# Kernel optimization log

Measured on AMD Instinct MI355X. Metric: run time of the kernel, lower is better.

The kernel has to match this reference:

```python
import jax, jax.numpy as jnp
import numpy as np

DIM, K_RANK, L, N_CLASS = 64, 16, 8, 10
H = 1e-3
B = 256
DD = DIM * DIM  # 4096


def _cay(C, D):
    # Cayley transform of B = C @ D^T : I + C (I - 0.5 D^T C)^{-1} D^T
    Id = jnp.eye(C.shape[1], dtype=C.dtype)
    DT = jnp.swapaxes(D, 1, 2)
    inv = jnp.linalg.inv(Id - 0.5 * DT @ C)
    return Id + C @ inv @ DT


def setup_inputs() -> dict:
    key = jax.random.key(0)
    ks = jax.random.split(key, 9)
    u = jax.random.normal(ks[0], (B, DIM, K_RANK), jnp.float32) / np.float32(np.sqrt(DIM))
    vh = jax.random.normal(ks[1], (B, K_RANK, DIM), jnp.float32) / np.float32(np.sqrt(DIM))
    eye_k = jnp.eye(K_RANK, dtype=jnp.float32)
    off = 0.05 * jax.random.normal(ks[2], (B, K_RANK, K_RANK), jnp.float32) * (1.0 - eye_k)
    dvals = jax.random.uniform(ks[3], (B, K_RANK), jnp.float32, 0.5, 1.5)
    s_core = off + dvals[:, :, None] * eye_k  # diag bounded away from 0 (invert_S)
    s_block = jnp.zeros((B, DIM, K_RANK), jnp.float32).at[:, :K_RANK, :K_RANK].set(s_core)
    X = jnp.stack([u.reshape(B, -1), s_block.reshape(B, -1), vh.reshape(B, -1)], axis=1)
    sc = np.float32(1.0 / np.sqrt(DD))
    W0 = sc * jax.random.normal(ks[4], (DD, DD), jnp.float32)
    W = sc * jax.random.normal(ks[5], (L, DD, DD), jnp.float32)
    b = sc * jax.random.normal(ks[6], (L, DD), jnp.float32)
    Wc = sc * jax.random.normal(ks[7], (N_CLASS, DD), jnp.float32)
    bc = sc * jax.random.normal(ks[8], (N_CLASS,), jnp.float32)
    return {"X": X, "W0": W0, "W": W, "b": b, "Wc": Wc, "bc": bc}


def reference(X, W0, W, b, Wc, bc):
    Bn = X.shape[0]
    u = X[:, 0].reshape(Bn, DIM, K_RANK)
    s = X[:, 1].reshape(Bn, DIM, K_RANK)[:, :K_RANK, :K_RANK]
    vh = X[:, 2].reshape(Bn, K_RANK, DIM)
    v = jnp.swapaxes(vh, 1, 2)
    eye_k = jnp.eye(K_RANK, dtype=X.dtype)
    eye_d = jnp.eye(DIM, dtype=X.dtype)
    Xf = (u @ s @ vh).reshape(Bn, DD)
    outs = []
    for i in range(L + 1):  # layer 0 has no bias
        lin = Xf @ W0.T if i == 0 else Xf @ W[i - 1].T + b[i - 1]
        dY = jax.nn.relu(lin).reshape(Bn, DIM, DIM)
        # invert_S: invert only the diagonal of s
        s_inv = (1.0 / jnp.diagonal(s, axis1=1, axis2=2))[:, :, None] * eye_k
        dU = dY @ v @ s_inv
        dV = jnp.swapaxes(dY, 1, 2) @ u @ jnp.swapaxes(s_inv, 1, 2)
        dS = jnp.swapaxes(u, 1, 2) @ dY @ v
        uT = jnp.swapaxes(u, 1, 2)
        F = (eye_d - u @ uT) @ dU
        FT = jnp.swapaxes(F, 1, 2)
        u = _cay(H * (F @ uT), -H * (u @ FT)) @ u
        vT = jnp.swapaxes(v, 1, 2)
        F = (eye_d - v @ vT) @ dV
        FT = jnp.swapaxes(F, 1, 2)
        v = _cay(H * (F @ vT), -H * (v @ FT)) @ v
        s = s + H * dS
        Xf = (u @ s @ jnp.swapaxes(v, 1, 2)).reshape(Bn, DD)
        outs.append(Xf)
    X_transformed = jnp.stack(outs, axis=-1)  # (B, dim*dim, L+1)
    X_classified = Xf @ Wc.T + bc
    X_predicted = jax.nn.softmax(X_classified, axis=1)
    return X_predicted, X_classified, X_transformed
```

## Files before the change

### kernel.cpp

```cpp
#include <hip/hip_runtime.h>
#include <math.h>

typedef unsigned short u16;
typedef unsigned int u32;
using bf16x8 = __attribute__((ext_vector_type(8))) short;
using f32x4  = __attribute__((ext_vector_type(4))) float;

#define DD 4096
#define NB 256
#define SPLIT_K 4
#define PSTRIDE (NB * DD)
#define PLANE (NB * DD)

__device__ __forceinline__ u16 f2bf(float f) {
  unsigned int u = __float_as_uint(f);
  u += 0x7fffu + ((u >> 16) & 1u);
  return (u16)(u >> 16);
}
__device__ __forceinline__ float bf2f(u16 h) {
  return __uint_as_float((u32)h << 16);
}
__device__ __forceinline__ unsigned int pack2bf(float a, float b) {
  return (unsigned int)f2bf(a) | ((unsigned int)f2bf(b) << 16);
}
__device__ __forceinline__ void async_cp16(const u16* g, u16* l) {
  __builtin_amdgcn_global_load_lds(
      (const __attribute__((address_space(1))) unsigned int*)g,
      (__attribute__((address_space(3))) unsigned int*)l, 16, 0, 0);
}
__device__ __forceinline__ float dot8bf(const uint4 a, const uint4 b) {
  float s;
  s  = __uint_as_float(a.x << 16) * __uint_as_float(b.x << 16);
  s += __uint_as_float(a.x & 0xffff0000u) * __uint_as_float(b.x & 0xffff0000u);
  s += __uint_as_float(a.y << 16) * __uint_as_float(b.y << 16);
  s += __uint_as_float(a.y & 0xffff0000u) * __uint_as_float(b.y & 0xffff0000u);
  s += __uint_as_float(a.z << 16) * __uint_as_float(b.z << 16);
  s += __uint_as_float(a.z & 0xffff0000u) * __uint_as_float(b.z & 0xffff0000u);
  s += __uint_as_float(a.w << 16) * __uint_as_float(b.w << 16);
  s += __uint_as_float(a.w & 0xffff0000u) * __uint_as_float(b.w & 0xffff0000u);
  return s;
}
__device__ __forceinline__ float dot4f(const float4 a, const float4 b) {
  return a.x * b.x + a.y * b.y + a.z * b.z + a.w * b.w;
}

__global__ __launch_bounds__(512, 8) void gemm_kernel(
    const u16* __restrict__ A, const float* __restrict__ W,
    u16* __restrict__ part)
{
  const int nt = blockIdx.x;
  const int mt = blockIdx.y & 1;
  const int kz = blockIdx.y >> 1;
  const int t = threadIdx.x;
  const int w = t >> 6, l = t & 63;

  __shared__ __align__(16) u16 As[128 * 64];
  __shared__ __align__(16) u16 Bs[64 * 64];

  const int colg0 = nt << 6;
  const int m0 = mt << 7;
  const int k0 = kz << 10;

  f32x4 acc[2][2];
#pragma unroll
  for (int mi = 0; mi < 2; ++mi)
#pragma unroll
    for (int nj = 0; nj < 2; ++nj)
      acc[mi][nj] = (f32x4){0.f, 0.f, 0.f, 0.f};

  const int wm = w & 3, wn = w >> 2;
  const int lr = l & 15, lg = l >> 4;
  const int arow_l = (w << 3) + (l >> 3);
  const int acl = l & 7;
  const int bn_l = t >> 3;
  const int bcc = t & 7;

  for (int tt = 0; tt < 16; ++tt) {
    const int kk = k0 + (tt << 6);
    __syncthreads();
#pragma unroll
    for (int r2 = 0; r2 < 2; ++r2) {
      const int row = (r2 << 6) + arow_l;
      const int cs = acl ^ (row & 7);
      async_cp16(A + ((size_t)(m0 + row) << 12) + kk + (cs << 3),
                 &As[(r2 << 12) + (w << 9)]);
    }
    {
      const float* wsrc = W + ((size_t)(colg0 + bn_l) << 12) + kk + (bcc << 3);
      const float4 f0 = *reinterpret_cast<const float4*>(wsrc);
      const float4 f1 = *reinterpret_cast<const float4*>(wsrc + 4);
      uint4 pk;
      pk.x = pack2bf(f0.x, f0.y);
      pk.y = pack2bf(f0.z, f0.w);
      pk.z = pack2bf(f1.x, f1.y);
      pk.w = pack2bf(f1.z, f1.w);
      *reinterpret_cast<uint4*>(&Bs[(bn_l << 6) + ((bcc ^ (bn_l & 7)) << 3)]) = pk;
    }
    __syncthreads();
#pragma unroll
    for (int ks = 0; ks < 2; ++ks) {
      const int cg = (ks << 2) + lg;
      bf16x8 av[2], bv[2];
#pragma unroll
      for (int mi = 0; mi < 2; ++mi) {
        const int fr = (wm << 5) + (mi << 4) + lr;
        av[mi] = *reinterpret_cast<const bf16x8*>(&As[(fr << 6) + ((cg ^ (fr & 7)) << 3)]);
      }
#pragma unroll
      for (int nj = 0; nj < 2; ++nj) {
        const int fc = (wn << 5) + (nj << 4) + lr;
        bv[nj] = *reinterpret_cast<const bf16x8*>(&Bs[(fc << 6) + ((cg ^ (fc & 7)) << 3)]);
      }
#pragma unroll
      for (int mi = 0; mi < 2; ++mi)
#pragma unroll
        for (int nj = 0; nj < 2; ++nj)
          acc[mi][nj] = __builtin_amdgcn_mfma_f32_16x16x32_bf16(
              av[mi], bv[nj], acc[mi][nj], 0, 0, 0);
    }
  }

  u16* pout = part + (size_t)kz * PSTRIDE;
#pragma unroll
  for (int mi = 0; mi < 2; ++mi)
#pragma unroll
    for (int nj = 0; nj < 2; ++nj) {
      const int col = colg0 + (wn << 5) + (nj << 4) + lr;
#pragma unroll
      for (int j = 0; j < 4; ++j) {
        const int row = m0 + (wm << 5) + (mi << 4) + (lg << 2) + j;
        pout[((size_t)row << 12) + col] = f2bf(acc[mi][nj][j]);
      }
    }
}

struct UpdSmem {
  float U[64][20], V[64][20], P[64][20];
  u16 UTb[16][72], VTb[16][72], PTb[16][72], QTb[16][72];
  float S[16][16], ST[16][16];
  float sinv[16];
  union {
    struct {
      u16 dYb[64][72];
      u16 dYTb[64][80];
    };
    struct {
      float Fu[64][20], Fv[64][20];
      u16 FuTb[16][72], FvTb[16][72];
      float R[16][20], RT[16][20], RvT[16][20];
      float G1u[16][20], G1v[16][20];
      float G2u[16][20], G2v[16][20];
      float M1uT[16][20], M1vT[16][20];
    };
  };
};

__device__ __forceinline__ void write_xf_tail(
    UpdSmem& m, int t, int b, float* __restrict__ Xf, u16* __restrict__ Xfb,
    float* __restrict__ outL_plane)
{
  const int p = t >> 3;
  const int j0 = (t << 1) & 15;
  {
    const float4* u4 = reinterpret_cast<const float4*>(&m.U[p][0]);
    const float4* sa = reinterpret_cast<const float4*>(&m.ST[j0][0]);
    const float4* sb = reinterpret_cast<const float4*>(&m.ST[j0 + 1][0]);
    float a0 = 0.f, a1 = 0.f;
#pragma unroll
    for (int k4 = 0; k4 < 4; ++k4) {
      const float4 uu = u4[k4];
      a0 += dot4f(uu, sa[k4]);
      a1 += dot4f(uu, sb[k4]);
    }
    m.P[p][j0] = a0; m.P[p][j0 + 1] = a1;
  }
  __syncthreads();
  {
    const int q0 = (t & 7) << 3;
    float4 pr[4];
    const float4* p4 = reinterpret_cast<const float4*>(&m.P[p][0]);
#pragma unroll
    for (int k4 = 0; k4 < 4; ++k4) pr[k4] = p4[k4];
    float res[8];
#pragma unroll
    for (int e = 0; e < 8; ++e) {
      const float4* v4 = reinterpret_cast<const float4*>(&m.V[q0 + e][0]);
      res[e] = dot4f(pr[0], v4[0]) + dot4f(pr[1], v4[1]) +
               dot4f(pr[2], v4[2]) + dot4f(pr[3], v4[3]);
    }
    const size_t ko = ((size_t)b << 12) + (p << 6) + q0;
    float4* xo = reinterpret_cast<float4*>(Xf + ko);
    const float4 r0 = make_float4(res[0], res[1], res[2], res[3]);
    const float4 r1 = make_float4(res[4], res[5], res[6], res[7]);
    xo[0] = r0; xo[1] = r1;
    uint4 pk;
    pk.x = pack2bf(res[0], res[1]); pk.y = pack2bf(res[2], res[3]);
    pk.z = pack2bf(res[4], res[5]); pk.w = pack2bf(res[6], res[7]);
    *reinterpret_cast<uint4*>(Xfb + ko) = pk;
    if (outL_plane != nullptr) {
      float4* op = reinterpret_cast<float4*>(outL_plane + ko);
      op[0] = r0; op[1] = r1;
    }
  }
}

__global__ __launch_bounds__(512) void update_kernel(
    const u16* __restrict__ part, const float* __restrict__ bias,
    float* __restrict__ u_g, float* __restrict__ v_g, float* __restrict__ s_g,
    float* __restrict__ Xf, u16* __restrict__ Xfb,
    float* __restrict__ outL, int layer)
{
  const int b = blockIdx.x, t = threadIdx.x;
  __shared__ __align__(16) UpdSmem m;
  float* outL_plane = outL + (size_t)layer * PLANE;
  const size_t ub = (size_t)b << 10;
  const int p8 = t >> 3;
  const int j0 = (t << 1) & 15;

  {
    const float2 u2 = *reinterpret_cast<const float2*>(u_g + ub + (t << 1));
    const float2 v2 = *reinterpret_cast<const float2*>(v_g + ub + (t << 1));
    const int r = t >> 3, c = (t & 7) << 1;
    m.U[r][c] = u2.x; m.U[r][c + 1] = u2.y;
    m.V[r][c] = v2.x; m.V[r][c + 1] = v2.y;
    m.UTb[c][r] = f2bf(u2.x); m.UTb[c + 1][r] = f2bf(u2.y);
    m.VTb[c][r] = f2bf(v2.x); m.VTb[c + 1][r] = f2bf(v2.y);
    if (t < 256) {
      const float sv = s_g[((size_t)b << 8) + t];
      m.S[t >> 4][t & 15] = sv;
      m.ST[t & 15][t >> 4] = sv;
    }
    if (t < 16) m.sinv[t] = 1.0f / s_g[((size_t)b << 8) + t * 17];
    const u16* p0 = part + ((size_t)b << 12) + (t << 3);
    float x[8];
#pragma unroll
    for (int e = 0; e < 8; ++e) x[e] = 0.f;
#pragma unroll
    for (int kzi = 0; kzi < SPLIT_K; ++kzi) {
      const uint4 v = *reinterpret_cast<const uint4*>(p0 + (size_t)kzi * PSTRIDE);
      x[0] += bf2f((u16)(v.x & 0xffff)); x[1] += bf2f((u16)(v.x >> 16));
      x[2] += bf2f((u16)(v.y & 0xffff)); x[3] += bf2f((u16)(v.y >> 16));
      x[4] += bf2f((u16)(v.z & 0xffff)); x[5] += bf2f((u16)(v.z >> 16));
      x[6] += bf2f((u16)(v.w & 0xffff)); x[7] += bf2f((u16)(v.w >> 16));
    }
    if (bias != nullptr) {
      const float4 b0 = *reinterpret_cast<const float4*>(bias + (t << 3));
      const float4 b1 = *reinterpret_cast<const float4*>(bias + (t << 3) + 4);
      x[0] += b0.x; x[1] += b0.y; x[2] += b0.z; x[3] += b0.w;
      x[4] += b1.x; x[5] += b1.y; x[6] += b1.z; x[7] += b1.w;
    }
#pragma unroll
    for (int e = 0; e < 8; ++e) x[e] = fmaxf(x[e], 0.f);
    const int r2 = t >> 3, c2 = (t & 7) << 3, sw = (t & 7) << 3;
    uint4 pk;
    pk.x = pack2bf(x[0], x[1]); pk.y = pack2bf(x[2], x[3]);
    pk.z = pack2bf(x[4], x[5]); pk.w = pack2bf(x[6], x[7]);
    *reinterpret_cast<uint4*>(&m.dYb[r2][c2]) = pk;
#pragma unroll
    for (int e = 0; e < 8; ++e) m.dYTb[c2 + e][r2 ^ sw] = f2bf(x[e]);
  }
  __syncthreads();

  {
    const int tt = t & 255;
    const int p = tt & 63, jg = (tt >> 6) << 2;
    float a[4] = {0.f, 0.f, 0.f, 0.f};
    if (t < 256) {
      const uint4* dy = reinterpret_cast<const uint4*>(&m.dYb[p][0]);
#pragma unroll
      for (int r8 = 0; r8 < 8; ++r8) {
        const uint4 d = dy[r8];
#pragma unroll
        for (int e = 0; e < 4; ++e)
          a[e] += dot8bf(d, reinterpret_cast<const uint4*>(&m.VTb[jg + e][0])[r8]);
      }
#pragma unroll
      for (int e = 0; e < 4; ++e) m.PTb[jg + e][p] = f2bf(a[e]);
    } else {
      const int sw = (p >> 3) & 7;
      const uint4* dy = reinterpret_cast<const uint4*>(&m.dYTb[p][0]);
#pragma unroll
      for (int r8 = 0; r8 < 8; ++r8) {
        const uint4 d = dy[r8 ^ sw];
#pragma unroll
        for (int e = 0; e < 4; ++e)
          a[e] += dot8bf(d, reinterpret_cast<const uint4*>(&m.UTb[jg + e][0])[r8]);
      }
#pragma unroll
      for (int e = 0; e < 4; ++e) m.QTb[jg + e][p] = f2bf(a[e]);
    }
  }
  __syncthreads();

  {
    const int tt = t & 255, i = tt >> 4, j = tt & 15;
    if (t < 256) {
      float r0 = 0.f, g0 = 0.f;
#pragma unroll
      for (int r8 = 0; r8 < 8; ++r8) {
        const uint4 ui = reinterpret_cast<const uint4*>(&m.UTb[i][0])[r8];
        r0 += dot8bf(ui, reinterpret_cast<const uint4*>(&m.PTb[j][0])[r8]);
        g0 += dot8bf(ui, reinterpret_cast<const uint4*>(&m.UTb[j][0])[r8]);
      }
      m.R[i][j] = r0; m.RT[j][i] = r0; m.G2u[i][j] = g0;
    } else {
      float r0 = 0.f, g0 = 0.f;
#pragma unroll
      for (int r8 = 0; r8 < 8; ++r8) {
        const uint4 vi = reinterpret_cast<const uint4*>(&m.VTb[i][0])[r8];
        r0 += dot8bf(vi, reinterpret_cast<const uint4*>(&m.QTb[j][0])[r8]);
        g0 += dot8bf(vi, reinterpret_cast<const uint4*>(&m.VTb[j][0])[r8]);
      }
      m.RvT[j][i] = r0; m.G2v[i][j] = g0;
    }
  }
  __syncthreads();

  {
    float f0 = bf2f(m.PTb[j0][p8]), f1 = bf2f(m.PTb[j0 + 1][p8]);
    float g0 = bf2f(m.QTb[j0][p8]), g1 = bf2f(m.QTb[j0 + 1][p8]);
    const float4* u4 = reinterpret_cast<const float4*>(&m.U[p8][0]);
    const float4* v4 = reinterpret_cast<const float4*>(&m.V[p8][0]);
    const float4* ra = reinterpret_cast<const float4*>(&m.RT[j0][0]);
    const float4* rb = reinterpret_cast<const float4*>(&m.RT[j0 + 1][0]);
    const float4* rc = reinterpret_cast<const float4*>(&m.RvT[j0][0]);
    const float4* rd = reinterpret_cast<const float4*>(&m.RvT[j0 + 1][0]);
#pragma unroll
    for (int k4 = 0; k4 < 4; ++k4) {
      const float4 uu = u4[k4], vv = v4[k4];
      f0 -= dot4f(uu, ra[k4]);
      f1 -= dot4f(uu, rb[k4]);
      g0 -= dot4f(vv, rc[k4]);
      g1 -= dot4f(vv, rd[k4]);
    }
    const float s0 = m.sinv[j0], s1 = m.sinv[j0 + 1];
    f0 *= s0; f1 *= s1; g0 *= s0; g1 *= s1;
    *reinterpret_cast<float2*>(&m.Fu[p8][j0]) = make_float2(f0, f1);
    *reinterpret_cast<float2*>(&m.Fv[p8][j0]) = make_float2(g0, g1);
    m.FuTb[j0][p8] = f2bf(f0); m.FuTb[j0 + 1][p8] = f2bf(f1);
    m.FvTb[j0][p8] = f2bf(g0); m.FvTb[j0 + 1][p8] = f2bf(g1);
  }
  __syncthreads();

  {
    const int tt = t & 255, i = tt >> 4, j = tt & 15;
    if (t < 256) {
      float g = 0.f;
#pragma unroll
      for (int r8 = 0; r8 < 8; ++r8)
        g += dot8bf(reinterpret_cast<const uint4*>(&m.UTb[i][0])[r8],
                    reinterpret_cast<const uint4*>(&m.FuTb[j][0])[r8]);
      m.G1u[i][j] = g;
    } else {
      float g = 0.f;
#pragma unroll
      for (int r8 = 0; r8 < 8; ++r8)
        g += dot8bf(reinterpret_cast<const uint4*>(&m.VTb[i][0])[r8],
                    reinterpret_cast<const uint4*>(&m.FvTb[j][0])[r8]);
      m.G1v[i][j] = g;
    }
  }
  __syncthreads();

  {
    const int tt = t & 255, i = tt >> 4, j = tt & 15;
    if (t < 256) {
      float mm = 0.f;
#pragma unroll
      for (int k4 = 0; k4 < 4; ++k4)
        mm += dot4f(reinterpret_cast<const float4*>(&m.G1u[i][0])[k4],
                    reinterpret_cast<const float4*>(&m.G2u[j][0])[k4]);
      m.M1uT[j][i] = mm;
    } else {
      float mm = 0.f;
#pragma unroll
      for (int k4 = 0; k4 < 4; ++k4)
        mm += dot4f(reinterpret_cast<const float4*>(&m.G1v[i][0])[k4],
                    reinterpret_cast<const float4*>(&m.G2v[j][0])[k4]);
      m.M1vT[j][i] = mm;
    }
  }
  __syncthreads();

  {
    float du0 = 0.f, du1 = 0.f, dv0 = 0.f, dv1 = 0.f;
    const float4* fu4 = reinterpret_cast<const float4*>(&m.Fu[p8][0]);
    const float4* fv4 = reinterpret_cast<const float4*>(&m.Fv[p8][0]);
    const float4* ma = reinterpret_cast<const float4*>(&m.M1uT[j0][0]);
    const float4* mb = reinterpret_cast<const float4*>(&m.M1uT[j0 + 1][0]);
    const float4* mc = reinterpret_cast<const float4*>(&m.M1vT[j0][0]);
    const float4* md = reinterpret_cast<const float4*>(&m.M1vT[j0 + 1][0]);
#pragma unroll
    for (int k4 = 0; k4 < 4; ++k4) {
      const float4 fu = fu4[k4], fv = fv4[k4];
      du0 += dot4f(fu, ma[k4]);
      du1 += dot4f(fu, mb[k4]);
      dv0 += dot4f(fv, mc[k4]);
      dv1 += dot4f(fv, md[k4]);
    }
    const float nu0 = m.U[p8][j0]     - 1e-6f * du0;
    const float nu1 = m.U[p8][j0 + 1] - 1e-6f * du1;
    const float nv0 = m.V[p8][j0]     - 1e-6f * dv0;
    const float nv1 = m.V[p8][j0 + 1] - 1e-6f * dv1;
    float ns = 0.f;
    if (t < 256) ns = m.S[t >> 4][t & 15] + 1e-3f * m.R[t >> 4][t & 15];
    __syncthreads();
    m.U[p8][j0] = nu0; m.U[p8][j0 + 1] = nu1;
    m.V[p8][j0] = nv0; m.V[p8][j0 + 1] = nv1;
    *reinterpret_cast<float2*>(u_g + ub + (p8 << 4) + j0) = make_float2(nu0, nu1);
    *reinterpret_cast<float2*>(v_g + ub + (p8 << 4) + j0) = make_float2(nv0, nv1);
    if (t < 256) {
      m.S[t >> 4][t & 15] = ns;
      m.ST[t & 15][t >> 4] = ns;
      s_g[((size_t)b << 8) + t] = ns;
    }
  }
  __syncthreads();

  write_xf_tail(m, t, b, Xf, Xfb, outL_plane);
}

__global__ __launch_bounds__(512) void init_kernel(
    const float* __restrict__ X, float* __restrict__ u_g, float* __restrict__ v_g,
    float* __restrict__ s_g, float* __restrict__ Xf, u16* __restrict__ Xfb)
{
  const int b = blockIdx.x, t = threadIdx.x;
  __shared__ __align__(16) UpdSmem m;
  const float* xb = X + (size_t)b * 3072;
  const size_t ub = (size_t)b << 10;
  {
    const float2 u2 = *reinterpret_cast<const float2*>(xb + (t << 1));
    const int r = t >> 3, c = (t & 7) << 1;
    m.U[r][c] = u2.x; m.U[r][c + 1] = u2.y;
    *reinterpret_cast<float2*>(u_g + ub + (t << 1)) = u2;
    if (t < 256) {
      const float sv = xb[1024 + t];
      m.S[t >> 4][t & 15] = sv;
      m.ST[t & 15][t >> 4] = sv;
      s_g[((size_t)b << 8) + t] = sv;
    }
    const float2 v2 = *reinterpret_cast<const float2*>(xb + 2048 + (t << 1));
    const int g2 = t << 1;
    const int iv = g2 >> 6, q = g2 & 63;
    m.V[q][iv] = v2.x; m.V[q + 1][iv] = v2.y;
    v_g[ub + (size_t)q * 16 + iv] = v2.x;
    v_g[ub + (size_t)(q + 1) * 16 + iv] = v2.y;
  }
  __syncthreads();
  write_xf_tail(m, t, b, Xf, Xfb, nullptr);
}

__global__ __launch_bounds__(256) void pack_cls_kernel(
    const float* __restrict__ outL, float* __restrict__ outT,
    const float* __restrict__ Xf, const float* __restrict__ Wc,
    const float* __restrict__ bc, float* __restrict__ pred,
    float* __restrict__ cls)
{
  const int t = threadIdx.x;
  const int bid = blockIdx.x;
  __shared__ float buf[256 * 9];
  __shared__ float red[4][10];
  {
    const int base = bid << 8;
#pragma unroll
    for (int l = 0; l < 9; ++l)
      buf[t * 9 + l] = outL[(size_t)l * PLANE + base + t];
    __syncthreads();
    const float4* b4 = reinterpret_cast<const float4*>(buf);
    float4* o4 = reinterpret_cast<float4*>(outT + (size_t)base * 9);
    for (int i = t; i < 576; i += 256) o4[i] = b4[i];
  }
  if (bid >= NB) return;
  const int b = bid;
  const int lane = t & 63, w = t >> 6;
  float acc[10];
#pragma unroll
  for (int c = 0; c < 10; ++c) acc[c] = 0.f;
  const float* xr = Xf + ((size_t)b << 12);
  for (int k = t; k < 4096; k += 256) {
    const float x = xr[k];
#pragma unroll
    for (int c = 0; c < 10; ++c) acc[c] += x * Wc[c * 4096 + k];
  }
#pragma unroll
  for (int c = 0; c < 10; ++c)
    for (int off = 32; off; off >>= 1) acc[c] += __shfl_xor(acc[c], off);
  if (lane == 0)
#pragma unroll
    for (int c = 0; c < 10; ++c) red[w][c] = acc[c];
  __syncthreads();
  if (t == 0) {
    float lg[10], ex[10];
    float mx = -1e30f;
#pragma unroll
    for (int c = 0; c < 10; ++c) {
      lg[c] = red[0][c] + red[1][c] + red[2][c] + red[3][c] + bc[c];
      mx = fmaxf(mx, lg[c]);
    }
    float s = 0.f;
#pragma unroll
    for (int c = 0; c < 10; ++c) { ex[c] = expf(lg[c] - mx); s += ex[c]; }
    const float inv = 1.f / s;
#pragma unroll
    for (int c = 0; c < 10; ++c) {
      cls[b * 10 + c] = lg[c];
      pred[b * 10 + c] = ex[c] * inv;
    }
  }
}

extern "C" void kernel_launch(void* const* d_in, const int* in_sizes, int n_in,
                              void* d_out, int out_size, void* d_ws, size_t ws_size,
                              hipStream_t stream) {
  (void)in_sizes; (void)n_in; (void)out_size; (void)ws_size;
  const float* X  = (const float*)d_in[0];
  const float* W0 = (const float*)d_in[1];
  const float* W  = (const float*)d_in[2];
  const float* bb = (const float*)d_in[3];
  const float* Wc = (const float*)d_in[4];
  const float* bc = (const float*)d_in[5];

  float* out_pred  = (float*)d_out;
  float* out_cls   = out_pred + 2560;
  float* out_trans = out_pred + 5120;

  char* ws = (char*)d_ws;
  float* Xf   = (float*)(ws);
  u16*   part = (u16*)  (ws + (4ull << 20));
  float* u_g  = (float*)(ws + (36ull << 20));
  float* v_g  = (float*)(ws + (37ull << 20));
  float* s_g  = (float*)(ws + (38ull << 20));
  u16*   Xfb  = (u16*)  (ws + (39ull << 20));
  float* outL = (float*)(ws + (41ull << 20));

  init_kernel<<<NB, 512, 0, stream>>>(X, u_g, v_g, s_g, Xf, Xfb);
  for (int i = 0; i <= 8; ++i) {
    const float* Wl = (i == 0) ? W0 : W + (size_t)(i - 1) * DD * DD;
    gemm_kernel<<<dim3(64, 2 * SPLIT_K), 512, 0, stream>>>(Xfb, Wl, part);
    update_kernel<<<NB, 512, 0, stream>>>(
        part, (i == 0) ? nullptr : (bb + (size_t)(i - 1) * DD),
        u_g, v_g, s_g, Xf, Xfb, outL, i);
  }
  pack_cls_kernel<<<4096, 256, 0, stream>>>(outL, out_trans, Xf, Wc, bc,
                                            out_pred, out_cls);
}
```

Measured before the change: 402.3 us.

## Double update and init kernel block size to 1024 threads and redistribute work

The per-batch update and init kernels now launch 1024 threads instead of 512. Work in each phase is split so that more threads run in parallel: U/V loading overlaps with the partial-sum reduction, the R/G2 products are spread over four groups, u and v updates go to separate halves, and the tail writes one float4 per thread. This cuts per-thread serial work in a latency-bound kernel with only 256 blocks, at the cost of more register pressure per block and some phases where half the threads sit idle.

New measurement: 399.1 us. About the same (-0.8%).

```diff
diff --git a/kernel.cpp b/kernel.cpp
--- a/kernel.cpp
+++ b/kernel.cpp
@@ -159,52 +159,41 @@
     UpdSmem& m, int t, int b, float* __restrict__ Xf, u16* __restrict__ Xfb,
     float* __restrict__ outL_plane)
 {
-  const int p = t >> 3;
-  const int j0 = (t << 1) & 15;
-  {
+  {
+    const int p = t >> 4, j = t & 15;
     const float4* u4 = reinterpret_cast<const float4*>(&m.U[p][0]);
-    const float4* sa = reinterpret_cast<const float4*>(&m.ST[j0][0]);
-    const float4* sb = reinterpret_cast<const float4*>(&m.ST[j0 + 1][0]);
-    float a0 = 0.f, a1 = 0.f;
-#pragma unroll
-    for (int k4 = 0; k4 < 4; ++k4) {
-      const float4 uu = u4[k4];
-      a0 += dot4f(uu, sa[k4]);
-      a1 += dot4f(uu, sb[k4]);
-    }
-    m.P[p][j0] = a0; m.P[p][j0 + 1] = a1;
-  }
-  __syncthreads();
-  {
-    const int q0 = (t & 7) << 3;
+    const float4* s4 = reinterpret_cast<const float4*>(&m.ST[j][0]);
+    float a = 0.f;
+#pragma unroll
+    for (int k4 = 0; k4 < 4; ++k4) a += dot4f(u4[k4], s4[k4]);
+    m.P[p][j] = a;
+  }
+  __syncthreads();
+  {
+    const int p = t >> 4, q0 = (t & 15) << 2;
     float4 pr[4];
     const float4* p4 = reinterpret_cast<const float4*>(&m.P[p][0]);
 #pragma unroll
     for (int k4 = 0; k4 < 4; ++k4) pr[k4] = p4[k4];
-    float res[8];
-#pragma unroll
-    for (int e = 0; e < 8; ++e) {
+    float res[4];
+#pragma unroll
+    for (int e = 0; e < 4; ++e) {
       const float4* v4 = reinterpret_cast<const float4*>(&m.V[q0 + e][0]);
       res[e] = dot4f(pr[0], v4[0]) + dot4f(pr[1], v4[1]) +
                dot4f(pr[2], v4[2]) + dot4f(pr[3], v4[3]);
     }
     const size_t ko = ((size_t)b << 12) + (p << 6) + q0;
-    float4* xo = reinterpret_cast<float4*>(Xf + ko);
     const float4 r0 = make_float4(res[0], res[1], res[2], res[3]);
-    const float4 r1 = make_float4(res[4], res[5], res[6], res[7]);
-    xo[0] = r0; xo[1] = r1;
-    uint4 pk;
+    *reinterpret_cast<float4*>(Xf + ko) = r0;
+    uint2 pk;
     pk.x = pack2bf(res[0], res[1]); pk.y = pack2bf(res[2], res[3]);
-    pk.z = pack2bf(res[4], res[5]); pk.w = pack2bf(res[6], res[7]);
-    *reinterpret_cast<uint4*>(Xfb + ko) = pk;
-    if (outL_plane != nullptr) {
-      float4* op = reinterpret_cast<float4*>(outL_plane + ko);
-      op[0] = r0; op[1] = r1;
-    }
-  }
-}
-
-__global__ __launch_bounds__(512) void update_kernel(
+    *reinterpret_cast<uint2*>(Xfb + ko) = pk;
+    if (outL_plane != nullptr)
+      *reinterpret_cast<float4*>(outL_plane + ko) = r0;
+  }
+}
+
+__global__ __launch_bounds__(1024) void update_kernel(
     const u16* __restrict__ part, const float* __restrict__ bias,
     float* __restrict__ u_g, float* __restrict__ v_g, float* __restrict__ s_g,
     float* __restrict__ Xf, u16* __restrict__ Xfb,
@@ -214,23 +203,8 @@
   __shared__ __align__(16) UpdSmem m;
   float* outL_plane = outL + (size_t)layer * PLANE;
   const size_t ub = (size_t)b << 10;
-  const int p8 = t >> 3;
-  const int j0 = (t << 1) & 15;
-
-  {
-    const float2 u2 = *reinterpret_cast<const float2*>(u_g + ub + (t << 1));
-    const float2 v2 = *reinterpret_cast<const float2*>(v_g + ub + (t << 1));
-    const int r = t >> 3, c = (t & 7) << 1;
-    m.U[r][c] = u2.x; m.U[r][c + 1] = u2.y;
-    m.V[r][c] = v2.x; m.V[r][c + 1] = v2.y;
-    m.UTb[c][r] = f2bf(u2.x); m.UTb[c + 1][r] = f2bf(u2.y);
-    m.VTb[c][r] = f2bf(v2.x); m.VTb[c + 1][r] = f2bf(v2.y);
-    if (t < 256) {
-      const float sv = s_g[((size_t)b << 8) + t];
-      m.S[t >> 4][t & 15] = sv;
-      m.ST[t & 15][t >> 4] = sv;
-    }
-    if (t < 16) m.sinv[t] = 1.0f / s_g[((size_t)b << 8) + t * 17];
+
+  if (t < 512) {
     const u16* p0 = part + ((size_t)b << 12) + (t << 3);
     float x[8];
 #pragma unroll
@@ -258,121 +232,147 @@
     *reinterpret_cast<uint4*>(&m.dYb[r2][c2]) = pk;
 #pragma unroll
     for (int e = 0; e < 8; ++e) m.dYTb[c2 + e][r2 ^ sw] = f2bf(x[e]);
-  }
-  __syncthreads();
-
-  {
-    const int tt = t & 255;
-    const int p = tt & 63, jg = (tt >> 6) << 2;
-    float a[4] = {0.f, 0.f, 0.f, 0.f};
-    if (t < 256) {
+  } else {
+    const int tq = t - 512;
+    const float2 u2 = *reinterpret_cast<const float2*>(u_g + ub + (tq << 1));
+    const float2 v2 = *reinterpret_cast<const float2*>(v_g + ub + (tq << 1));
+    const int r = tq >> 3, c = (tq & 7) << 1;
+    m.U[r][c] = u2.x; m.U[r][c + 1] = u2.y;
+    m.V[r][c] = v2.x; m.V[r][c + 1] = v2.y;
+    m.UTb[c][r] = f2bf(u2.x); m.UTb[c + 1][r] = f2bf(u2.y);
+    m.VTb[c][r] = f2bf(v2.x); m.VTb[c + 1][r] = f2bf(v2.y);
+    if (tq < 256) {
+      const float sv = s_g[((size_t)b << 8) + tq];
+      m.S[tq >> 4][tq & 15] = sv;
+      m.ST[tq & 15][tq >> 4] = sv;
+    }
+    if (tq < 16) m.sinv[tq] = 1.0f / s_g[((size_t)b << 8) + tq * 17];
+  }
+  __syncthreads();
+
+  {
+    const int h = t >> 9, tq = t & 511;
+    const int p = tq & 63, j0 = (tq >> 6) << 1;
+    float a0 = 0.f, a1 = 0.f;
+    if (h == 0) {
       const uint4* dy = reinterpret_cast<const uint4*>(&m.dYb[p][0]);
 #pragma unroll
       for (int r8 = 0; r8 < 8; ++r8) {
         const uint4 d = dy[r8];
-#pragma unroll
-        for (int e = 0; e < 4; ++e)
-          a[e] += dot8bf(d, reinterpret_cast<const uint4*>(&m.VTb[jg + e][0])[r8]);
-      }
-#pragma unroll
-      for (int e = 0; e < 4; ++e) m.PTb[jg + e][p] = f2bf(a[e]);
+        a0 += dot8bf(d, reinterpret_cast<const uint4*>(&m.VTb[j0][0])[r8]);
+        a1 += dot8bf(d, reinterpret_cast<const uint4*>(&m.VTb[j0 + 1][0])[r8]);
+      }
+      m.PTb[j0][p] = f2bf(a0); m.PTb[j0 + 1][p] = f2bf(a1);
     } else {
       const int sw = (p >> 3) & 7;
       const uint4* dy = reinterpret_cast<const uint4*>(&m.dYTb[p][0]);
 #pragma unroll
       for (int r8 = 0; r8 < 8; ++r8) {
         const uint4 d = dy[r8 ^ sw];
-#pragma unroll
-        for (int e = 0; e < 4; ++e)
-          a[e] += dot8bf(d, reinterpret_cast<const uint4*>(&m.UTb[jg + e][0])[r8]);
-      }
-#pragma unroll
-      for (int e = 0; e < 4; ++e) m.QTb[jg + e][p] = f2bf(a[e]);
-    }
-  }
-  __syncthreads();
-
-  {
-    const int tt = t & 255, i = tt >> 4, j = tt & 15;
-    if (t < 256) {
-      float r0 = 0.f, g0 = 0.f;
-#pragma unroll
-      for (int r8 = 0; r8 < 8; ++r8) {
-        const uint4 ui = reinterpret_cast<const uint4*>(&m.UTb[i][0])[r8];
-        r0 += dot8bf(ui, reinterpret_cast<const uint4*>(&m.PTb[j][0])[r8]);
-        g0 += dot8bf(ui, reinterpret_cast<const uint4*>(&m.UTb[j][0])[r8]);
-      }
-      m.R[i][j] = r0; m.RT[j][i] = r0; m.G2u[i][j] = g0;
-    } else {
-      float r0 = 0.f, g0 = 0.f;
-#pragma unroll
-      for (int r8 = 0; r8 < 8; ++r8) {
-        const uint4 vi = reinterpret_cast<const uint4*>(&m.VTb[i][0])[r8];
-        r0 += dot8bf(vi, reinterpret_cast<const uint4*>(&m.QTb[j][0])[r8]);
-        g0 += dot8bf(vi, reinterpret_cast<const uint4*>(&m.VTb[j][0])[r8]);
-      }
-      m.RvT[j][i] = r0; m.G2v[i][j] = g0;
-    }
-  }
-  __syncthreads();
-
-  {
-    float f0 = bf2f(m.PTb[j0][p8]), f1 = bf2f(m.PTb[j0 + 1][p8]);
-    float g0 = bf2f(m.QTb[j0][p8]), g1 = bf2f(m.QTb[j0 + 1][p8]);
-    const float4* u4 = reinterpret_cast<const float4*>(&m.U[p8][0]);
-    const float4* v4 = reinterpret_cast<const float4*>(&m.V[p8][0]);
-    const float4* ra = reinterpret_cast<const float4*>(&m.RT[j0][0]);
-    const float4* rb = reinterpret_cast<const float4*>(&m.RT[j0 + 1][0]);
-    const float4* rc = reinterpret_cast<const float4*>(&m.RvT[j0][0]);
-    const float4* rd = reinterpret_cast<const float4*>(&m.RvT[j0 + 1][0]);
-#pragma unroll
-    for (int k4 = 0; k4 < 4; ++k4) {
-      const float4 uu = u4[k4], vv = v4[k4];
-      f0 -= dot4f(uu, ra[k4]);
-      f1 -= dot4f(uu, rb[k4]);
-      g0 -= dot4f(vv, rc[k4]);
-      g1 -= dot4f(vv, rd[k4]);
-    }
+        a0 += dot8bf(d, reinterpret_cast<const uint4*>(&m.UTb[j0][0])[r8]);
+        a1 += dot8bf(d, reinterpret_cast<const uint4*>(&m.UTb[j0 + 1][0])[r8]);
+      }
+      m.QTb[j0][p] = f2bf(a0); m.QTb[j0 + 1][p] = f2bf(a1);
+    }
+  }
+  __syncthreads();
+
+  {
+    const int g = t >> 8, tq = t & 255, i = tq >> 4, j = tq & 15;
+    float s = 0.f;
+    if (g == 0) {
+#pragma unroll
+      for (int r8 = 0; r8 < 8; ++r8)
+        s += dot8bf(reinterpret_cast<const uint4*>(&m.UTb[i][0])[r8],
+                    reinterpret_cast<const uint4*>(&m.PTb[j][0])[r8]);
+      m.R[i][j] = s; m.RT[j][i] = s;
+    } else if (g == 1) {
+#pragma unroll
+      for (int r8 = 0; r8 < 8; ++r8)
+        s += dot8bf(reinterpret_cast<const uint4*>(&m.UTb[i][0])[r8],
+                    reinterpret_cast<const uint4*>(&m.UTb[j][0])[r8]);
+      m.G2u[i][j] = s;
+    } else if (g == 2) {
+#pragma unroll
+      for (int r8 = 0; r8 < 8; ++r8)
+        s += dot8bf(reinterpret_cast<const uint4*>(&m.VTb[i][0])[r8],
+                    reinterpret_cast<const uint4*>(&m.QTb[j][0])[r8]);
+      m.RvT[j][i] = s;
+    } else {
+#pragma unroll
+      for (int r8 = 0; r8 < 8; ++r8)
+        s += dot8bf(reinterpret_cast<const uint4*>(&m.VTb[i][0])[r8],
+                    reinterpret_cast<const uint4*>(&m.VTb[j][0])[r8]);
+      m.G2v[i][j] = s;
+    }
+  }
+  __syncthreads();
+
+  {
+    const int h = t >> 9, tq = t & 511;
+    const int p8 = tq >> 3, j0 = (tq << 1) & 15;
     const float s0 = m.sinv[j0], s1 = m.sinv[j0 + 1];
-    f0 *= s0; f1 *= s1; g0 *= s0; g1 *= s1;
-    *reinterpret_cast<float2*>(&m.Fu[p8][j0]) = make_float2(f0, f1);
-    *reinterpret_cast<float2*>(&m.Fv[p8][j0]) = make_float2(g0, g1);
-    m.FuTb[j0][p8] = f2bf(f0); m.FuTb[j0 + 1][p8] = f2bf(f1);
-    m.FvTb[j0][p8] = f2bf(g0); m.FvTb[j0 + 1][p8] = f2bf(g1);
-  }
-  __syncthreads();
-
-  {
-    const int tt = t & 255, i = tt >> 4, j = tt & 15;
-    if (t < 256) {
-      float g = 0.f;
+    if (h == 0) {
+      float f0 = bf2f(m.PTb[j0][p8]), f1 = bf2f(m.PTb[j0 + 1][p8]);
+      const float4* u4 = reinterpret_cast<const float4*>(&m.U[p8][0]);
+      const float4* ra = reinterpret_cast<const float4*>(&m.RT[j0][0]);
+      const float4* rb = reinterpret_cast<const float4*>(&m.RT[j0 + 1][0]);
+#pragma unroll
+      for (int k4 = 0; k4 < 4; ++k4) {
+        const float4 uu = u4[k4];
+        f0 -= dot4f(uu, ra[k4]);
+        f1 -= dot4f(uu, rb[k4]);
+      }
+      f0 *= s0; f1 *= s1;
+      *reinterpret_cast<float2*>(&m.Fu[p8][j0]) = make_float2(f0, f1);
+      m.FuTb[j0][p8] = f2bf(f0); m.FuTb[j0 + 1][p8] = f2bf(f1);
+    } else {
+      float g0 = bf2f(m.QTb[j0][p8]), g1 = bf2f(m.QTb[j0 + 1][p8]);
+      const float4* v4 = reinterpret_cast<const float4*>(&m.V[p8][0]);
+      const float4* rc = reinterpret_cast<const float4*>(&m.RvT[j0][0]);
+      const float4* rd = reinterpret_cast<const float4*>(&m.RvT[j0 + 1][0]);
+#pragma unroll
+      for (int k4 = 0; k4 < 4; ++k4) {
+        const float4 vv = v4[k4];
+        g0 -= dot4f(vv, rc[k4]);
+        g1 -= dot4f(vv, rd[k4]);
+      }
+      g0 *= s0; g1 *= s1;
+      *reinterpret_cast<float2*>(&m.Fv[p8][j0]) = make_float2(g0, g1);
+      m.FvTb[j0][p8] = f2bf(g0); m.FvTb[j0 + 1][p8] = f2bf(g1);
+    }
+  }
+  __syncthreads();
+
+  if (t < 512) {
+    const int g = t >> 8, tq = t & 255, i = tq >> 4, j = tq & 15;
+    float s = 0.f;
+    if (g == 0) {
 #pragma unroll
       for (int r8 = 0; r8 < 8; ++r8)
-        g += dot8bf(reinterpret_cast<const uint4*>(&m.UTb[i][0])[r8],
+        s += dot8bf(reinterpret_cast<const uint4*>(&m.UTb[i][0])[r8],
                     reinterpret_cast<const uint4*>(&m.FuTb[j][0])[r8]);
-      m.G1u[i][j] = g;
-    } else {
-      float g = 0.f;
+      m.G1u[i][j] = s;
+    } else {
 #pragma unroll
       for (int r8 = 0; r8 < 8; ++r8)
-        g += dot8bf(reinterpret_cast<const uint4*>(&m.VTb[i][0])[r8],
+        s += dot8bf(reinterpret_cast<const uint4*>(&m.VTb[i][0])[r8],
                     reinterpret_cast<const uint4*>(&m.FvTb[j][0])[r8]);
-      m.G1v[i][j] = g;
-    }
-  }
-  __syncthreads();
-
-  {
-    const int tt = t & 255, i = tt >> 4, j = tt & 15;
-    if (t < 256) {
-      float mm = 0.f;
+      m.G1v[i][j] = s;
+    }
+  }
+  __syncthreads();
+
+  if (t < 512) {
+    const int g = t >> 8, tq = t & 255, i = tq >> 4, j = tq & 15;
+    float mm = 0.f;
+    if (g == 0) {
 #pragma unroll
       for (int k4 = 0; k4 < 4; ++k4)
         mm += dot4f(reinterpret_cast<const float4*>(&m.G1u[i][0])[k4],
                     reinterpret_cast<const float4*>(&m.G2u[j][0])[k4]);
       m.M1uT[j][i] = mm;
     } else {
-      float mm = 0.f;
 #pragma unroll
       for (int k4 = 0; k4 < 4; ++k4)
         mm += dot4f(reinterpret_cast<const float4*>(&m.G1v[i][0])[k4],
@@ -383,36 +383,49 @@
   __syncthreads();
 
   {
-    float du0 = 0.f, du1 = 0.f, dv0 = 0.f, dv1 = 0.f;
-    const float4* fu4 = reinterpret_cast<const float4*>(&m.Fu[p8][0]);
-    const float4* fv4 = reinterpret_cast<const float4*>(&m.Fv[p8][0]);
-    const float4* ma = reinterpret_cast<const float4*>(&m.M1uT[j0][0]);
-    const float4* mb = reinterpret_cast<const float4*>(&m.M1uT[j0 + 1][0]);
-    const float4* mc = reinterpret_cast<const float4*>(&m.M1vT[j0][0]);
-    const float4* md = reinterpret_cast<const float4*>(&m.M1vT[j0 + 1][0]);
-#pragma unroll
-    for (int k4 = 0; k4 < 4; ++k4) {
-      const float4 fu = fu4[k4], fv = fv4[k4];
-      du0 += dot4f(fu, ma[k4]);
-      du1 += dot4f(fu, mb[k4]);
-      dv0 += dot4f(fv, mc[k4]);
-      dv1 += dot4f(fv, md[k4]);
-    }
-    const float nu0 = m.U[p8][j0]     - 1e-6f * du0;
-    const float nu1 = m.U[p8][j0 + 1] - 1e-6f * du1;
-    const float nv0 = m.V[p8][j0]     - 1e-6f * dv0;
-    const float nv1 = m.V[p8][j0 + 1] - 1e-6f * dv1;
-    float ns = 0.f;
-    if (t < 256) ns = m.S[t >> 4][t & 15] + 1e-3f * m.R[t >> 4][t & 15];
+    const int h = t >> 9, tq = t & 511;
+    const int p8 = tq >> 3, j0 = (tq << 1) & 15;
+    float n0, n1, ns = 0.f;
+    if (h == 0) {
+      float du0 = 0.f, du1 = 0.f;
+      const float4* fu4 = reinterpret_cast<const float4*>(&m.Fu[p8][0]);
+      const float4* ma = reinterpret_cast<const float4*>(&m.M1uT[j0][0]);
+      const float4* mb = reinterpret_cast<const float4*>(&m.M1uT[j0 + 1][0]);
+#pragma unroll
+      for (int k4 = 0; k4 < 4; ++k4) {
+        const float4 fu = fu4[k4];
+        du0 += dot4f(fu, ma[k4]);
+        du1 += dot4f(fu, mb[k4]);
+      }
+      n0 = m.U[p8][j0]     - 1e-6f * du0;
+      n1 = m.U[p8][j0 + 1] - 1e-6f * du1;
+    } else {
+      float dv0 = 0.f, dv1 = 0.f;
+      const float4* fv4 = reinterpret_cast<const float4*>(&m.Fv[p8][0]);
+      const float4* mc = reinterpret_cast<const float4*>(&m.M1vT[j0][0]);
+      const float4* md = reinterpret_cast<const float4*>(&m.M1vT[j0 + 1][0]);
+#pragma unroll
+      for (int k4 = 0; k4 < 4; ++k4) {
+        const float4 fv = fv4[k4];
+        dv0 += dot4f(fv, mc[k4]);
+        dv1 += dot4f(fv, md[k4]);
+      }
+      n0 = m.V[p8][j0]     - 1e-6f * dv0;
+      n1 = m.V[p8][j0 + 1] - 1e-6f * dv1;
+      if (tq < 256) ns = m.S[tq >> 4][tq & 15] + 1e-3f * m.R[tq >> 4][tq & 15];
+    }
     __syncthreads();
-    m.U[p8][j0] = nu0; m.U[p8][j0 + 1] = nu1;
-    m.V[p8][j0] = nv0; m.V[p8][j0 + 1] = nv1;
-    *reinterpret_cast<float2*>(u_g + ub + (p8 << 4) + j0) = make_float2(nu0, nu1);
-    *reinterpret_cast<float2*>(v_g + ub + (p8 << 4) + j0) = make_float2(nv0, nv1);
-    if (t < 256) {
-      m.S[t >> 4][t & 15] = ns;
-      m.ST[t & 15][t >> 4] = ns;
-      s_g[((size_t)b << 8) + t] = ns;
+    if (h == 0) {
+      m.U[p8][j0] = n0; m.U[p8][j0 + 1] = n1;
+      *reinterpret_cast<float2*>(u_g + ub + (p8 << 4) + j0) = make_float2(n0, n1);
+    } else {
+      m.V[p8][j0] = n0; m.V[p8][j0 + 1] = n1;
+      *reinterpret_cast<float2*>(v_g + ub + (p8 << 4) + j0) = make_float2(n0, n1);
+      if (tq < 256) {
+        m.S[tq >> 4][tq & 15] = ns;
+        m.ST[tq & 15][tq >> 4] = ns;
+        s_g[((size_t)b << 8) + tq] = ns;
+      }
     }
   }
   __syncthreads();
@@ -420,7 +433,7 @@
   write_xf_tail(m, t, b, Xf, Xfb, outL_plane);
 }
 
-__global__ __launch_bounds__(512) void init_kernel(
+__global__ __launch_bounds__(1024) void init_kernel(
     const float* __restrict__ X, float* __restrict__ u_g, float* __restrict__ v_g,
     float* __restrict__ s_g, float* __restrict__ Xf, u16* __restrict__ Xfb)
 {
@@ -428,23 +441,25 @@
   __shared__ __align__(16) UpdSmem m;
   const float* xb = X + (size_t)b * 3072;
   const size_t ub = (size_t)b << 10;
-  {
+  if (t < 512) {
     const float2 u2 = *reinterpret_cast<const float2*>(xb + (t << 1));
     const int r = t >> 3, c = (t & 7) << 1;
     m.U[r][c] = u2.x; m.U[r][c + 1] = u2.y;
     *reinterpret_cast<float2*>(u_g + ub + (t << 1)) = u2;
-    if (t < 256) {
-      const float sv = xb[1024 + t];
-      m.S[t >> 4][t & 15] = sv;
-      m.ST[t & 15][t >> 4] = sv;
-      s_g[((size_t)b << 8) + t] = sv;
-    }
-    const float2 v2 = *reinterpret_cast<const float2*>(xb + 2048 + (t << 1));
-    const int g2 = t << 1;
+  } else {
+    const int tq = t - 512;
+    const float2 v2 = *reinterpret_cast<const float2*>(xb + 2048 + (tq << 1));
+    const int g2 = tq << 1;
     const int iv = g2 >> 6, q = g2 & 63;
     m.V[q][iv] = v2.x; m.V[q + 1][iv] = v2.y;
     v_g[ub + (size_t)q * 16 + iv] = v2.x;
     v_g[ub + (size_t)(q + 1) * 16 + iv] = v2.y;
+    if (tq < 256) {
+      const float sv = xb[1024 + tq];
+      m.S[tq >> 4][tq & 15] = sv;
+      m.ST[tq & 15][tq >> 4] = sv;
+      s_g[((size_t)b << 8) + tq] = sv;
+    }
   }
   __syncthreads();
   write_xf_tail(m, t, b, Xf, Xfb, nullptr);
@@ -533,11 +548,11 @@
   u16*   Xfb  = (u16*)  (ws + (39ull << 20));
   float* outL = (float*)(ws + (41ull << 20));
 
-  init_kernel<<<NB, 512, 0, stream>>>(X, u_g, v_g, s_g, Xf, Xfb);
+  init_kernel<<<NB, 1024, 0, stream>>>(X, u_g, v_g, s_g, Xf, Xfb);
   for (int i = 0; i <= 8; ++i) {
     const float* Wl = (i == 0) ? W0 : W + (size_t)(i - 1) * DD * DD;
     gemm_kernel<<<dim3(64, 2 * SPLIT_K), 512, 0, stream>>>(Xfb, Wl, part);
-    update_kernel<<<NB, 512, 0, stream>>>(
+    update_kernel<<<NB, 1024, 0, stream>>>(
         part, (i == 0) ? nullptr : (bb + (size_t)(i - 1) * DD),
         u_g, v_g, s_g, Xf, Xfb, outL, i);
   }
```
